# Kernel optimization log

Measured on AMD Instinct MI355X. Metric: run time of the kernel, lower is better.

## Reference

```python
import jax, jax.numpy as jnp
import numpy as np

N = 4096      # mesh nodes (seq len)
D = 512       # input_dim_nodes / hidden_size
F = 512       # ffn_hidden_size (hidden_dim)
NH = 4        # num_attention_heads
HD = D // NH  # head dim = 128
L = 2         # processor_layers
EPS = 1e-5
SCALE = 1.0 / float(np.sqrt(HD))
NEG = -1e9


def setup_inputs() -> dict:
    key = jax.random.key(0)
    ks = jax.random.split(key, 16)
    nfeat = jax.random.normal(ks[0], (N, D), jnp.float32)
    # sparse graph adjacency mask: True = masked out (TE 'arbitrary' convention)
    mask = jax.random.uniform(ks[1], (N, N)) < 0.99
    idx = jnp.arange(N)
    mask = mask.at[idx, idx].set(False)  # keep self-edges unmasked
    s = 0.02
    p = lambda k, shape: jax.random.normal(k, shape, jnp.float32) * s
    return dict(
        nfeat=nfeat, mask=mask,
        ln1_g=jnp.ones((L, D), jnp.float32), ln1_b=jnp.zeros((L, D), jnp.float32),
        wq=p(ks[2], (L, D, D)), bq=p(ks[3], (L, D)),
        wk=p(ks[4], (L, D, D)), bk=p(ks[5], (L, D)),
        wv=p(ks[6], (L, D, D)), bv=p(ks[7], (L, D)),
        wo=p(ks[8], (L, D, D)), bo=p(ks[9], (L, D)),
        ln2_g=jnp.ones((L, D), jnp.float32), ln2_b=jnp.zeros((L, D), jnp.float32),
        fc1_w=p(ks[10], (L, F, D)), fc1_b=p(ks[11], (L, F)),
        fc2_w=p(ks[12], (L, D, F)), fc2_b=p(ks[13], (L, D)),
    )


def _ln(x, g, b):
    mu = x.mean(-1, keepdims=True)
    var = ((x - mu) ** 2).mean(-1, keepdims=True)
    return (x - mu) * jax.lax.rsqrt(var + EPS) * g + b


def reference(nfeat, mask, ln1_g, ln1_b, wq, bq, wk, bk, wv, bv, wo, bo,
              ln2_g, ln2_b, fc1_w, fc1_b, fc2_w, fc2_b):
    def layer(x, p):
        g1, b1, Wq, Bq, Wk, Bk, Wv, Bv, Wo, Bo, g2, b2, W1, B1, W2, B2 = p
        # --- pre-LN self-attention with arbitrary mask ---
        h = _ln(x, g1, b1)                                  # [N, D]
        q = (h @ Wq.T + Bq).reshape(N, NH, HD)
        k = (h @ Wk.T + Bk).reshape(N, NH, HD)
        v = (h @ Wv.T + Bv).reshape(N, NH, HD)
        scores = jnp.einsum('qhd,khd->hqk', q, k) * SCALE   # [NH, N, N]
        scores = jnp.where(mask[None], NEG, scores)
        attn = jax.nn.softmax(scores, axis=-1)
        o = jnp.einsum('hqk,khd->qhd', attn, v).reshape(N, D)
        x = x + o @ Wo.T + Bo
        # --- pre-LN MLP ---
        h2 = _ln(x, g2, b2)
        m = jax.nn.gelu(h2 @ W1.T + B1, approximate=False) @ W2.T + B2
        return x + m, None

    xs = (ln1_g, ln1_b, wq, bq, wk, bk, wv, bv, wo, bo,
          ln2_g, ln2_b, fc1_w, fc1_b, fc2_w, fc2_b)
    out, _ = jax.lax.scan(layer, nfeat, xs)
    return out
```

## Files before the change

### kernel.cpp

```cpp
#include <hip/hip_runtime.h>
#include <math.h>

#define NN 4096
#define DD 512
#define FF 512
#define CAP 256
#define SCALE 0.08838834764831845f

typedef unsigned short u16;
typedef unsigned char u8;
typedef __attribute__((ext_vector_type(8))) short short8;
typedef __attribute__((ext_vector_type(8))) unsigned short ushort8;
typedef __attribute__((ext_vector_type(4))) unsigned short ushort4v;
typedef __attribute__((ext_vector_type(4))) float floatx4;
typedef __attribute__((ext_vector_type(2))) float f32x2;
typedef _Float16 half8v __attribute__((ext_vector_type(8)));

__device__ __forceinline__ float bf2f(u16 u) {
    union { unsigned int i; float f; } x; x.i = ((unsigned int)u) << 16; return x.f;
}
__device__ __forceinline__ u16 f2bf(float f) {
    union { float f; unsigned int i; } x; x.f = f;
    unsigned int r = (x.i + 0x7FFFu + ((x.i >> 16) & 1u)) >> 16;
    return (u16)r;
}
__device__ __forceinline__ u16 f2h(float f) {
    _Float16 h = (_Float16)f;
    union { _Float16 h; u16 u; } x; x.h = h; return x.u;
}
__device__ __forceinline__ u8 f2fp8(float f) {
    union { _Float16 h; u16 u; } x;
    x.h = (_Float16)(f * 0.00390625f);
    u16 h = x.u;
    h = h + 0x3F + ((h >> 7) & 1);
    return (u8)(((h >> 8) & 0x80) | ((h >> 7) & 0x7f));
}
__device__ __forceinline__ float fp82f_sw(u8 b) {
    union { u16 u; _Float16 h; } x;
    x.u = (u16)(((u16)(b & 0x80) << 8) | ((u16)(b & 0x7f) << 7));
    return (float)x.h * 256.0f;
}
__device__ __forceinline__ void gld_lds16(const void* g, void* l) {
    __builtin_amdgcn_global_load_lds((const __attribute__((address_space(1))) void*)g,
                                     (__attribute__((address_space(3))) void*)l, 16, 0, 0);
}

struct W6 {
    const float* w[6];
    const float* bq; const float* bk; const float* bv;
};
__global__ void setup_kernel(W6 wp, u16* __restrict__ dst, float* __restrict__ bcat,
                             const int* __restrict__ mask, int* __restrict__ idx,
                             int* __restrict__ cnt) {
    __shared__ int c;
    if (blockIdx.x >= 192) {
        int row = blockIdx.x - 192;
        if (threadIdx.x == 0) c = 0;
        __syncthreads();
        const int4* mrow = (const int4*)(mask + (size_t)row * NN);
        for (int j4 = threadIdx.x; j4 < NN / 4; j4 += blockDim.x) {
            int4 m4 = mrow[j4];
            int base = j4 * 4;
            if (m4.x == 0) idx[row * CAP + atomicAdd(&c, 1)] = base;
            if (m4.y == 0) idx[row * CAP + atomicAdd(&c, 1)] = base + 1;
            if (m4.z == 0) idx[row * CAP + atomicAdd(&c, 1)] = base + 2;
            if (m4.w == 0) idx[row * CAP + atomicAdd(&c, 1)] = base + 3;
        }
        __syncthreads();
        if (threadIdx.x == 0) cnt[row] = (c < CAP) ? c : CAP;
        return;
    }
    int region = blockIdx.x >> 4;
    int layer = region / 6, mat = region - layer * 6;
    const float* src = wp.w[mat] + (size_t)layer * (DD * DD);
    u16* d = dst + (size_t)region * (DD * DD);
    int off = (blockIdx.x & 15) * 16384 + threadIdx.x * 4;
#pragma unroll
    for (int i = 0; i < 16; i++) {
        int e = off + i * 1024;
        float4 f = *(const float4*)&src[e];
        ushort4v u;
        u.x = f2bf(f.x); u.y = f2bf(f.y); u.z = f2bf(f.z); u.w = f2bf(f.w);
        *(ushort4v*)&d[e] = u;
    }
    if (blockIdx.x < 2) {
        int l = blockIdx.x;
        for (int it = 0; it < 6; it++) {
            int j = it * 256 + threadIdx.x;
            int m = j >> 9, col = j & 511;
            const float* bp = (m == 0) ? wp.bq : (m == 1) ? wp.bk : wp.bv;
            bcat[l * 1536 + j] = bp[l * DD + col];
        }
    }
}

__global__ void ln_kernel(const float* __restrict__ x, const float* __restrict__ g,
                          const float* __restrict__ b, u16* __restrict__ out) {
    int wave = threadIdx.x >> 6, lane = threadIdx.x & 63;
    int row = blockIdx.x * 4 + wave;
    const float* xr = x + (size_t)row * DD;
    float4 p0 = *(const float4*)&xr[lane * 8];
    float4 p1 = *(const float4*)&xr[lane * 8 + 4];
    float v[8] = {p0.x, p0.y, p0.z, p0.w, p1.x, p1.y, p1.z, p1.w};
    float s = 0.f;
#pragma unroll
    for (int i = 0; i < 8; i++) s += v[i];
#pragma unroll
    for (int off = 32; off; off >>= 1) s += __shfl_xor(s, off);
    float mu = s * (1.0f / DD);
    float vs = 0.f;
#pragma unroll
    for (int i = 0; i < 8; i++) { float d = v[i] - mu; vs += d * d; }
#pragma unroll
    for (int off = 32; off; off >>= 1) vs += __shfl_xor(vs, off);
    float r = rsqrtf(vs * (1.0f / DD) + 1e-5f);
    float4 g0 = *(const float4*)&g[lane * 8];
    float4 g1 = *(const float4*)&g[lane * 8 + 4];
    float4 b0 = *(const float4*)&b[lane * 8];
    float4 b1 = *(const float4*)&b[lane * 8 + 4];
    float ge[8] = {g0.x, g0.y, g0.z, g0.w, g1.x, g1.y, g1.z, g1.w};
    float be[8] = {b0.x, b0.y, b0.z, b0.w, b1.x, b1.y, b1.z, b1.w};
    ushort8 ov;
#pragma unroll
    for (int i = 0; i < 8; i++) ov[i] = f2bf((v[i] - mu) * r * ge[i] + be[i]);
    *(ushort8*)&out[(size_t)row * DD + lane * 8] = ov;
}

__device__ __forceinline__ float gelu_fast(float val) {
    float z = fabsf(val) * 0.70710678118654752f;
    float tt = __builtin_amdgcn_rcpf(fmaf(0.3275911f, z, 1.0f));
    float p = fmaf(1.061405429f, tt, -1.453152027f);
    p = fmaf(p, tt, 1.421413741f);
    p = fmaf(p, tt, -0.284496736f);
    p = fmaf(p, tt, 0.254829592f);
    p = p * tt * __expf(-z * z);
    float er_ = 1.0f - p;
    float sgn = (val < 0.f) ? -er_ : er_;
    return val * 0.5f * (1.0f + sgn);
}


template <int MODE>
__launch_bounds__(256)
__global__ void gemm_bf16(const u16* __restrict__ A, const u16* __restrict__ B,
                          const float* __restrict__ bias, const float* __restrict__ resIn,
                          float* __restrict__ resOut, u16* __restrict__ outB,
                          int M, int Nout, int K) {
    __shared__ u16 As[2 * 64 * 64];
    __shared__ u16 Bs[2 * 64 * 64];
    const int m0 = blockIdx.y * 64, n0 = blockIdx.x * 64;
    const int t = threadIdx.x;
    const int wave = t >> 6, lane = t & 63;
    const int wm = (wave & 1) * 32, wn = (wave >> 1) * 32;
    const int sr = t >> 3;
    const int sc = ((((t & 7) - (t >> 3)) & 7)) * 8;
    const int fr = lane & 15, g0 = lane >> 4;
    const int er = (lane >> 4) * 4, ec = lane & 15;

    floatx4 acc[2][2] = {};
    const u16* ag0 = A + (size_t)(m0 + sr) * K + sc;
    const u16* ag1 = A + (size_t)(m0 + 32 + sr) * K + sc;
    const u16* bg0 = B + (size_t)(n0 + sr) * K + sc;
    const u16* bg1 = B + (size_t)(n0 + 32 + sr) * K + sc;
    u16* as0 = As + t * 8;
    u16* as1 = As + 32 * 64 + t * 8;
    u16* bs0 = Bs + t * 8;
    u16* bs1 = Bs + 32 * 64 + t * 8;

    float rin[16];
    if (MODE == 2) {
#pragma unroll
        for (int i = 0; i < 2; i++)
#pragma unroll
            for (int j = 0; j < 2; j++)
#pragma unroll
                for (int r = 0; r < 4; r++)
                    rin[(i * 2 + j) * 4 + r] =
                        resIn[(size_t)(m0 + wm + 16 * i + er + r) * Nout + (n0 + wn + 16 * j + ec)];
    }

    auto stage = [&](int buf, int k0) {
        int o = buf * 4096;
        gld_lds16(ag0 + k0, as0 + o);
        gld_lds16(ag1 + k0, as1 + o);
        gld_lds16(bg0 + k0, bs0 + o);
        gld_lds16(bg1 + k0, bs1 + o);
    };

    const int NK = K >> 6;
    stage(0, 0);
    int cur = 0;
    for (int kt = 0; kt < NK; kt++) {
        __syncthreads();
        if (kt + 1 < NK) stage(cur ^ 1, (kt + 1) * 64);
        const u16* Ab = As + cur * 4096;
        const u16* Bb = Bs + cur * 4096;
#pragma unroll
        for (int h = 0; h < 2; h++) {
            const int fo = (((h << 2) + g0 + fr) & 7) << 3;
            short8 af[2], bf[2];
#pragma unroll
            for (int i = 0; i < 2; i++) af[i] = *(const short8*)&Ab[(wm + 16 * i + fr) * 64 + fo];
#pragma unroll
            for (int j = 0; j < 2; j++) bf[j] = *(const short8*)&Bb[(wn + 16 * j + fr) * 64 + fo];
#pragma unroll
            for (int i = 0; i < 2; i++)
#pragma unroll
                for (int j = 0; j < 2; j++)
                    acc[i][j] = __builtin_amdgcn_mfma_f32_16x16x32_bf16(af[i], bf[j], acc[i][j], 0, 0, 0);
        }
        cur ^= 1;
    }

#pragma unroll
    for (int i = 0; i < 2; i++) {
#pragma unroll
        for (int j = 0; j < 2; j++) {
            int col = n0 + wn + 16 * j + ec;
            float bsv = bias[col];
#pragma unroll
            for (int r = 0; r < 4; r++) {
                int row = m0 + wm + 16 * i + er + r;
                float val = acc[i][j][r] + bsv;
                if (MODE == 1) val = gelu_fast(val);
                if (MODE == 2) {
                    resOut[(size_t)row * Nout + col] = rin[(i * 2 + j) * 4 + r] + val;
                } else {
                    outB[(size_t)row * Nout + col] = f2bf(val);
                }
            }
        }
    }
}

__launch_bounds__(256)
__global__ void gemm_qkv(const u16* __restrict__ A, const u16* __restrict__ B,
                         const float* __restrict__ bias, u16* __restrict__ qOut,
                         u8* __restrict__ kv8) {
    __shared__ u16 As[2 * 128 * 64];
    __shared__ u16 Bs[2 * 64 * 64];
    const int m0 = blockIdx.y * 128, n0 = blockIdx.x * 64;
    const int t = threadIdx.x;
    const int wave = t >> 6, lane = t & 63;
    const int wm = (wave & 1) * 64, wn = (wave >> 1) * 32;
    const int sr = t >> 3;
    const int sc = ((((t & 7) - (t >> 3)) & 7)) * 8;
    const int fr = lane & 15, g0 = lane >> 4;

    floatx4 acc[4][2] = {};
    const u16* agp[4];
    u16* asp[4];
#pragma unroll
    for (int u = 0; u < 4; u++) {
        agp[u] = A + (size_t)(m0 + 32 * u + sr) * DD + sc;
        asp[u] = As + u * (32 * 64) + t * 8;
    }
    const u16* bg0 = B + (size_t)(n0 + sr) * DD + sc;
    const u16* bg1 = B + (size_t)(n0 + 32 + sr) * DD + sc;
    u16* bs0 = Bs + t * 8;
    u16* bs1 = Bs + 32 * 64 + t * 8;

    auto stage = [&](int buf, int k0) {
        int oa = buf * 8192, ob = buf * 4096;
#pragma unroll
        for (int u = 0; u < 4; u++) gld_lds16(agp[u] + k0, asp[u] + oa);
        gld_lds16(bg0 + k0, bs0 + ob);
        gld_lds16(bg1 + k0, bs1 + ob);
    };

    stage(0, 0);
    int cur = 0;
    for (int kt = 0; kt < 8; kt++) {
        __syncthreads();
        if (kt + 1 < 8) stage(cur ^ 1, (kt + 1) * 64);
        const u16* Ab = As + cur * 8192;
        const u16* Bb = Bs + cur * 4096;
#pragma unroll
        for (int h = 0; h < 2; h++) {
            const int fo = (((h << 2) + g0 + fr) & 7) << 3;
            short8 af[4], bf[2];
#pragma unroll
            for (int i = 0; i < 4; i++) af[i] = *(const short8*)&Ab[(wm + 16 * i + fr) * 64 + fo];
#pragma unroll
            for (int j = 0; j < 2; j++) bf[j] = *(const short8*)&Bb[(wn + 16 * j + fr) * 64 + fo];
#pragma unroll
            for (int i = 0; i < 4; i++)
#pragma unroll
                for (int j = 0; j < 2; j++)
                    acc[i][j] = __builtin_amdgcn_mfma_f32_16x16x32_bf16(af[i], bf[j], acc[i][j], 0, 0, 0);
        }
        cur ^= 1;
    }

    const int er = (lane >> 4) * 4, ec = lane & 15;
    const int bx = blockIdx.x;
#pragma unroll
    for (int j = 0; j < 2; j++) {
        int col = n0 + wn + 16 * j + ec;
        float bsv = bias[col];
#pragma unroll
        for (int i = 0; i < 4; i++) {
#pragma unroll
            for (int r = 0; r < 4; r++) {
                int row = m0 + wm + 16 * i + er + r;
                float val = acc[i][j][r] + bsv;
                if (bx < 8) {
                    qOut[(size_t)row * 512 + col] = f2h(val);
                } else if (bx < 16) {
                    int cc = col - 512;
                    kv8[(size_t)row * 1024 + 16 * (cc >> 3) + (cc & 7)] = f2fp8(val);
                } else {
                    int cc = col - 1024;
                    kv8[(size_t)row * 1024 + 16 * (cc >> 3) + 8 + (cc & 7)] = f2fp8(val);
                }
            }
        }
    }
}

__global__ void sparse_attn(const u16* __restrict__ q, const u8* __restrict__ kv8,
                            const int* __restrict__ idx, const int* __restrict__ cnt,
                            u16* __restrict__ o) {
    int t = threadIdx.x;
    int wave = t >> 6, lane = t & 63;
    int qslot = wave >> 1, half = wave & 1;
    int qi = blockIdx.x * 4 + qslot;
    __shared__ float obuf[4][64][8];
    __shared__ float sbuf[4][64];
    __shared__ int sidx[4][CAP];

    int c = cnt[qi];
    const int* ir = idx + qi * CAP;
    for (int j = t & 127; j < c; j += 128) sidx[qslot][j] = ir[j];

    half8v qv = *(const half8v*)(q + (size_t)qi * 512 + lane * 8);
    float qf[8];
#pragma unroll
    for (int e = 0; e < 8; e++) qf[e] = (float)qv[e];
    __syncthreads();

    float sum = 0.f, oa[8] = {};
    int j = half;
    int4 kv0, kv1;
    {
        int k0i = (j < c) ? sidx[qslot][j] : 0;
        int k1i = (j + 2 < c) ? sidx[qslot][j + 2] : 0;
        kv0 = *(const int4*)(kv8 + (size_t)k0i * 1024 + lane * 16);
        kv1 = *(const int4*)(kv8 + (size_t)k1i * 1024 + lane * 16);
    }
    while (j < c) {
        int4 kvn;
        {
            int kjn = (j + 4 < c) ? sidx[qslot][j + 4] : 0;
            kvn = *(const int4*)(kv8 + (size_t)kjn * 1024 + lane * 16);
        }
        float kd[8], vd[8];
#if __has_builtin(__builtin_amdgcn_cvt_pk_f32_fp8)
        {
            f32x2 p0 = __builtin_amdgcn_cvt_pk_f32_fp8(kv0.x, false);
            f32x2 p1 = __builtin_amdgcn_cvt_pk_f32_fp8(kv0.x, true);
            f32x2 p2 = __builtin_amdgcn_cvt_pk_f32_fp8(kv0.y, false);
            f32x2 p3 = __builtin_amdgcn_cvt_pk_f32_fp8(kv0.y, true);
            kd[0] = p0.x; kd[1] = p0.y; kd[2] = p1.x; kd[3] = p1.y;
            kd[4] = p2.x; kd[5] = p2.y; kd[6] = p3.x; kd[7] = p3.y;
            f32x2 p4 = __builtin_amdgcn_cvt_pk_f32_fp8(kv0.z, false);
            f32x2 p5 = __builtin_amdgcn_cvt_pk_f32_fp8(kv0.z, true);
            f32x2 p6 = __builtin_amdgcn_cvt_pk_f32_fp8(kv0.w, false);
            f32x2 p7 = __builtin_amdgcn_cvt_pk_f32_fp8(kv0.w, true);
            vd[0] = p4.x; vd[1] = p4.y; vd[2] = p5.x; vd[3] = p5.y;
            vd[4] = p6.x; vd[5] = p6.y; vd[6] = p7.x; vd[7] = p7.y;
        }
#else
        {
            const u8* bp = (const u8*)&kv0;
#pragma unroll
            for (int e = 0; e < 8; e++) { kd[e] = fp82f_sw(bp[e]); vd[e] = fp82f_sw(bp[8 + e]); }
        }
#endif
        float d = 0.f;
#pragma unroll
        for (int e = 0; e < 8; e++) d = fmaf(qf[e], kd[e], d);
        d += __shfl_xor(d, 1);
        d += __shfl_xor(d, 2);
        d += __shfl_xor(d, 4);
        d += __shfl_xor(d, 8);
        float p = __expf(d * SCALE);
        sum += p;
#pragma unroll
        for (int e = 0; e < 8; e++) oa[e] = fmaf(p, vd[e], oa[e]);
        kv0 = kv1;
        kv1 = kvn;
        j += 2;
    }

    if (half == 1) {
#pragma unroll
        for (int e = 0; e < 8; e++) obuf[qslot][lane][e] = oa[e];
        sbuf[qslot][lane] = sum;
    }
    __syncthreads();
    if (half == 0) {
        sum += sbuf[qslot][lane];
        float inv = 1.0f / sum;
        ushort8 ov;
#pragma unroll
        for (int e = 0; e < 8; e++) ov[e] = f2bf((oa[e] + obuf[qslot][lane][e]) * inv);
        *(ushort8*)(o + (size_t)qi * 512 + lane * 8) = ov;
    }
}

extern "C" void kernel_launch(void* const* d_in, const int* in_sizes, int n_in,
                              void* d_out, int out_size, void* d_ws, size_t ws_size,
                              hipStream_t stream) {
    const float* nfeat = (const float*)d_in[0];
    const int*   mask  = (const int*)d_in[1];
    const float* ln1_g = (const float*)d_in[2];
    const float* ln1_b = (const float*)d_in[3];
    const float* bo    = (const float*)d_in[11];
    const float* ln2_g = (const float*)d_in[12];
    const float* ln2_b = (const float*)d_in[13];
    const float* fc1_b = (const float*)d_in[15];
    const float* fc2_b = (const float*)d_in[17];

    const size_t ND = (size_t)NN * DD;
    float* x    = (float*)d_ws;
    u16*   h    = (u16*)(x + ND);
    u16*   q    = h + ND;
    u8*    kv8  = (u8*)(q + ND);
    u16*   o    = (u16*)(kv8 + (size_t)NN * 1024);
    u16*   m1   = o + ND;
    u16*   wc   = m1 + ND;
    float* bcat = (float*)(wc + (size_t)12 * DD * DD);
    int*   idx  = (int*)(bcat + 2 * 1536);
    int*   cnt  = idx + (size_t)NN * CAP;

    W6 w6;
    w6.w[0] = (const float*)d_in[4];  w6.w[1] = (const float*)d_in[6];
    w6.w[2] = (const float*)d_in[8];  w6.w[3] = (const float*)d_in[10];
    w6.w[4] = (const float*)d_in[14]; w6.w[5] = (const float*)d_in[16];
    w6.bq = (const float*)d_in[5]; w6.bk = (const float*)d_in[7]; w6.bv = (const float*)d_in[9];
    setup_kernel<<<192 + NN, 256, 0, stream>>>(w6, wc, bcat, mask, idx, cnt);

    const size_t SS = (size_t)DD * DD;
    for (int l = 0; l < 2; l++) {
        size_t bOff = (size_t)l * DD;
        u16* wl = wc + (size_t)l * 6 * SS;
        const float* xin = (l == 0) ? nfeat : x;
        float* fc2_dst = (l == 1) ? (float*)d_out : x;

        ln_kernel<<<NN / 4, 256, 0, stream>>>(xin, ln1_g + bOff, ln1_b + bOff, h);
        gemm_qkv<<<dim3(24, 32), 256, 0, stream>>>(h, wl, bcat + l * 1536, q, kv8);
        sparse_attn<<<NN / 4, 512, 0, stream>>>(q, kv8, idx, cnt, o);
        gemm_bf16<2><<<dim3(8, 64), 256, 0, stream>>>(o, wl + 3 * SS, bo + bOff,
                                                      xin, x, nullptr, NN, DD, DD);
        ln_kernel<<<NN / 4, 256, 0, stream>>>(x, ln2_g + bOff, ln2_b + bOff, h);
        gemm_bf16<1><<<dim3(8, 64), 256, 0, stream>>>(h, wl + 4 * SS, fc1_b + bOff,
                                                      nullptr, nullptr, m1, NN, FF, DD);
        gemm_bf16<2><<<dim3(8, 64), 256, 0, stream>>>(m1, wl + 5 * SS, fc2_b + bOff,
                                                      x, fc2_dst, nullptr, NN, DD, FF);
    }
}
```

Before: 281.4 us.

## Fuse LayerNorm into GEMM prologues using row statistics accumulated in epilogues

Removes the standalone LayerNorm kernels. Per-row sum and sum-of-squares are now computed in the setup kernel for the input and atomically accumulated in the residual GEMM epilogues. The QKV and FC1 GEMMs then normalize fp32 activations on the fly while staging the A tile into LDS, which removes the bf16 h round trip and two launches per layer. In exchange, the A tile moves from async global-to-LDS loads to register loads at twice the bytes, the epilogues gain LDS reductions and atomics, and one-pass variance (E[x²]-mu²) may lose some precision.

```diff
diff --git a/kernel.cpp b/kernel.cpp
--- a/kernel.cpp
+++ b/kernel.cpp
@@ -43,87 +43,6 @@
 __device__ __forceinline__ void gld_lds16(const void* g, void* l) {
     __builtin_amdgcn_global_load_lds((const __attribute__((address_space(1))) void*)g,
                                      (__attribute__((address_space(3))) void*)l, 16, 0, 0);
-}
-
-struct W6 {
-    const float* w[6];
-    const float* bq; const float* bk; const float* bv;
-};
-__global__ void setup_kernel(W6 wp, u16* __restrict__ dst, float* __restrict__ bcat,
-                             const int* __restrict__ mask, int* __restrict__ idx,
-                             int* __restrict__ cnt) {
-    __shared__ int c;
-    if (blockIdx.x >= 192) {
-        int row = blockIdx.x - 192;
-        if (threadIdx.x == 0) c = 0;
-        __syncthreads();
-        const int4* mrow = (const int4*)(mask + (size_t)row * NN);
-        for (int j4 = threadIdx.x; j4 < NN / 4; j4 += blockDim.x) {
-            int4 m4 = mrow[j4];
-            int base = j4 * 4;
-            if (m4.x == 0) idx[row * CAP + atomicAdd(&c, 1)] = base;
-            if (m4.y == 0) idx[row * CAP + atomicAdd(&c, 1)] = base + 1;
-            if (m4.z == 0) idx[row * CAP + atomicAdd(&c, 1)] = base + 2;
-            if (m4.w == 0) idx[row * CAP + atomicAdd(&c, 1)] = base + 3;
-        }
-        __syncthreads();
-        if (threadIdx.x == 0) cnt[row] = (c < CAP) ? c : CAP;
-        return;
-    }
-    int region = blockIdx.x >> 4;
-    int layer = region / 6, mat = region - layer * 6;
-    const float* src = wp.w[mat] + (size_t)layer * (DD * DD);
-    u16* d = dst + (size_t)region * (DD * DD);
-    int off = (blockIdx.x & 15) * 16384 + threadIdx.x * 4;
-#pragma unroll
-    for (int i = 0; i < 16; i++) {
-        int e = off + i * 1024;
-        float4 f = *(const float4*)&src[e];
-        ushort4v u;
-        u.x = f2bf(f.x); u.y = f2bf(f.y); u.z = f2bf(f.z); u.w = f2bf(f.w);
-        *(ushort4v*)&d[e] = u;
-    }
-    if (blockIdx.x < 2) {
-        int l = blockIdx.x;
-        for (int it = 0; it < 6; it++) {
-            int j = it * 256 + threadIdx.x;
-            int m = j >> 9, col = j & 511;
-            const float* bp = (m == 0) ? wp.bq : (m == 1) ? wp.bk : wp.bv;
-            bcat[l * 1536 + j] = bp[l * DD + col];
-        }
-    }
-}
-
-__global__ void ln_kernel(const float* __restrict__ x, const float* __restrict__ g,
-                          const float* __restrict__ b, u16* __restrict__ out) {
-    int wave = threadIdx.x >> 6, lane = threadIdx.x & 63;
-    int row = blockIdx.x * 4 + wave;
-    const float* xr = x + (size_t)row * DD;
-    float4 p0 = *(const float4*)&xr[lane * 8];
-    float4 p1 = *(const float4*)&xr[lane * 8 + 4];
-    float v[8] = {p0.x, p0.y, p0.z, p0.w, p1.x, p1.y, p1.z, p1.w};
-    float s = 0.f;
-#pragma unroll
-    for (int i = 0; i < 8; i++) s += v[i];
-#pragma unroll
-    for (int off = 32; off; off >>= 1) s += __shfl_xor(s, off);
-    float mu = s * (1.0f / DD);
-    float vs = 0.f;
-#pragma unroll
-    for (int i = 0; i < 8; i++) { float d = v[i] - mu; vs += d * d; }
-#pragma unroll
-    for (int off = 32; off; off >>= 1) vs += __shfl_xor(vs, off);
-    float r = rsqrtf(vs * (1.0f / DD) + 1e-5f);
-    float4 g0 = *(const float4*)&g[lane * 8];
-    float4 g1 = *(const float4*)&g[lane * 8 + 4];
-    float4 b0 = *(const float4*)&b[lane * 8];
-    float4 b1 = *(const float4*)&b[lane * 8 + 4];
-    float ge[8] = {g0.x, g0.y, g0.z, g0.w, g1.x, g1.y, g1.z, g1.w};
-    float be[8] = {b0.x, b0.y, b0.z, b0.w, b1.x, b1.y, b1.z, b1.w};
-    ushort8 ov;
-#pragma unroll
-    for (int i = 0; i < 8; i++) ov[i] = f2bf((v[i] - mu) * r * ge[i] + be[i]);
-    *(ushort8*)&out[(size_t)row * DD + lane * 8] = ov;
 }
 
 __device__ __forceinline__ float gelu_fast(float val) {
@@ -139,13 +58,84 @@
     return val * 0.5f * (1.0f + sgn);
 }
 
-
-template <int MODE>
+struct W6 {
+    const float* w[6];
+    const float* bq; const float* bk; const float* bv;
+};
+__global__ void setup_kernel(W6 wp, u16* __restrict__ dst, float* __restrict__ bcat,
+                             const int* __restrict__ mask, int* __restrict__ idx,
+                             int* __restrict__ cnt, const float* __restrict__ nfeat,
+                             float* __restrict__ st) {
+    __shared__ int c;
+    const int bid = blockIdx.x;
+    if (bid >= 192 + NN) {
+        int wave = threadIdx.x >> 6, lane = threadIdx.x & 63;
+        int row = (bid - 192 - NN) * 4 + wave;
+        const float* xr = nfeat + (size_t)row * DD + lane * 8;
+        float4 a = *(const float4*)xr;
+        float4 b4 = *(const float4*)(xr + 4);
+        float v[8] = {a.x, a.y, a.z, a.w, b4.x, b4.y, b4.z, b4.w};
+        float s1 = 0.f, s2 = 0.f;
+#pragma unroll
+        for (int e = 0; e < 8; e++) { s1 += v[e]; s2 += v[e] * v[e]; }
+#pragma unroll
+        for (int off = 32; off; off >>= 1) { s1 += __shfl_xor(s1, off); s2 += __shfl_xor(s2, off); }
+        if (lane == 0) { st[row * 2] = s1; st[row * 2 + 1] = s2; }
+        return;
+    }
+    if (bid >= 192) {
+        int row = bid - 192;
+        if (threadIdx.x == 0) c = 0;
+        __syncthreads();
+        const int4* mrow = (const int4*)(mask + (size_t)row * NN);
+        for (int j4 = threadIdx.x; j4 < NN / 4; j4 += blockDim.x) {
+            int4 m4 = mrow[j4];
+            int base = j4 * 4;
+            if (m4.x == 0) idx[row * CAP + atomicAdd(&c, 1)] = base;
+            if (m4.y == 0) idx[row * CAP + atomicAdd(&c, 1)] = base + 1;
+            if (m4.z == 0) idx[row * CAP + atomicAdd(&c, 1)] = base + 2;
+            if (m4.w == 0) idx[row * CAP + atomicAdd(&c, 1)] = base + 3;
+        }
+        __syncthreads();
+        if (threadIdx.x == 0) cnt[row] = (c < CAP) ? c : CAP;
+        return;
+    }
+    int region = bid >> 4;
+    int layer = region / 6, mat = region - layer * 6;
+    const float* src = wp.w[mat] + (size_t)layer * (DD * DD);
+    u16* d = dst + (size_t)region * (DD * DD);
+    int off = (bid & 15) * 16384 + threadIdx.x * 4;
+#pragma unroll
+    for (int i = 0; i < 16; i++) {
+        int e = off + i * 1024;
+        float4 f = *(const float4*)&src[e];
+        ushort4v u;
+        u.x = f2bf(f.x); u.y = f2bf(f.y); u.z = f2bf(f.z); u.w = f2bf(f.w);
+        *(ushort4v*)&d[e] = u;
+    }
+    if (bid < 2) {
+        int l = bid;
+        for (int it = 0; it < 6; it++) {
+            int j = it * 256 + threadIdx.x;
+            int m = j >> 9, col = j & 511;
+            const float* bp = (m == 0) ? wp.bq : (m == 1) ? wp.bk : wp.bv;
+            bcat[l * 1536 + j] = bp[l * DD + col];
+        }
+    }
+    if (bid == 2 || bid == 3) {
+        float* z = st + 8192;
+        int base = (bid - 2) * 256 + threadIdx.x;
+#pragma unroll
+        for (int i = 0; i < 48; i++) z[base + i * 512] = 0.0f;
+    }
+}
+
+
 __launch_bounds__(256)
-__global__ void gemm_bf16(const u16* __restrict__ A, const u16* __restrict__ B,
-                          const float* __restrict__ bias, const float* __restrict__ resIn,
-                          float* __restrict__ resOut, u16* __restrict__ outB,
-                          int M, int Nout, int K) {
+__global__ void gemm_res(const u16* __restrict__ A, const u16* __restrict__ B,
+                         const float* __restrict__ bias, const float* __restrict__ resIn,
+                         float* __restrict__ resOut, float* __restrict__ statsOut,
+                         int Nout, int K) {
     __shared__ u16 As[2 * 64 * 64];
     __shared__ u16 Bs[2 * 64 * 64];
     const int m0 = blockIdx.y * 64, n0 = blockIdx.x * 64;
@@ -168,16 +158,14 @@
     u16* bs1 = Bs + 32 * 64 + t * 8;
 
     float rin[16];
-    if (MODE == 2) {
-#pragma unroll
-        for (int i = 0; i < 2; i++)
-#pragma unroll
-            for (int j = 0; j < 2; j++)
-#pragma unroll
-                for (int r = 0; r < 4; r++)
-                    rin[(i * 2 + j) * 4 + r] =
-                        resIn[(size_t)(m0 + wm + 16 * i + er + r) * Nout + (n0 + wn + 16 * j + ec)];
-    }
+#pragma unroll
+    for (int i = 0; i < 2; i++)
+#pragma unroll
+        for (int j = 0; j < 2; j++)
+#pragma unroll
+            for (int r = 0; r < 4; r++)
+                rin[(i * 2 + j) * 4 + r] =
+                    resIn[(size_t)(m0 + wm + 16 * i + er + r) * Nout + (n0 + wn + 16 * j + ec)];
 
     auto stage = [&](int buf, int k0) {
         int o = buf * 4096;
@@ -212,6 +200,7 @@
         cur ^= 1;
     }
 
+    float outv[16];
 #pragma unroll
     for (int i = 0; i < 2; i++) {
 #pragma unroll
@@ -221,22 +210,161 @@
 #pragma unroll
             for (int r = 0; r < 4; r++) {
                 int row = m0 + wm + 16 * i + er + r;
-                float val = acc[i][j][r] + bsv;
-                if (MODE == 1) val = gelu_fast(val);
-                if (MODE == 2) {
-                    resOut[(size_t)row * Nout + col] = rin[(i * 2 + j) * 4 + r] + val;
-                } else {
-                    outB[(size_t)row * Nout + col] = f2bf(val);
-                }
+                float val = rin[(i * 2 + j) * 4 + r] + acc[i][j][r] + bsv;
+                outv[(i * 2 + j) * 4 + r] = val;
+                resOut[(size_t)row * Nout + col] = val;
             }
         }
     }
+
+    if (statsOut) {
+        __syncthreads();
+        float* Ls = (float*)As;
+#pragma unroll
+        for (int i = 0; i < 2; i++)
+#pragma unroll
+            for (int j = 0; j < 2; j++)
+#pragma unroll
+                for (int r = 0; r < 4; r++)
+                    Ls[(wm + 16 * i + er + r) * 64 + (wn + 16 * j + ec)] = outv[(i * 2 + j) * 4 + r];
+        __syncthreads();
+        if (t < 64) {
+            float s1 = 0.f, s2 = 0.f;
+            for (int c0 = 0; c0 < 64; c0++) {
+                int cc = (c0 + t) & 63;
+                float v = Ls[t * 64 + cc];
+                s1 += v; s2 += v * v;
+            }
+            atomicAdd(&statsOut[(size_t)(m0 + t) * 2], s1);
+            atomicAdd(&statsOut[(size_t)(m0 + t) * 2 + 1], s2);
+        }
+    }
 }
 
 __launch_bounds__(256)
-__global__ void gemm_qkv(const u16* __restrict__ A, const u16* __restrict__ B,
-                         const float* __restrict__ bias, u16* __restrict__ qOut,
-                         u8* __restrict__ kv8) {
+__global__ void gemm_ln_gelu(const float* __restrict__ X, const float* __restrict__ stats,
+                             const float* __restrict__ lg, const float* __restrict__ lb,
+                             const u16* __restrict__ B, const float* __restrict__ bias,
+                             u16* __restrict__ outB) {
+    __shared__ u16 As[2 * 64 * 64];
+    __shared__ u16 Bs[2 * 64 * 64];
+    const int m0 = blockIdx.y * 64, n0 = blockIdx.x * 64;
+    const int t = threadIdx.x;
+    const int wave = t >> 6, lane = t & 63;
+    const int wm = (wave & 1) * 32, wn = (wave >> 1) * 32;
+    const int sr = t >> 3;
+    const int sc = ((((t & 7) - (t >> 3)) & 7)) * 8;
+    const int fr = lane & 15, g0 = lane >> 4;
+
+    floatx4 acc[2][2] = {};
+    const float* xp0 = X + (size_t)(m0 + sr) * DD + sc;
+    const float* xp1 = X + (size_t)(m0 + 32 + sr) * DD + sc;
+    float mu0, r0, mu1, r1;
+    {
+        int ra = m0 + sr, rb = m0 + 32 + sr;
+        float s1 = stats[ra * 2], s2 = stats[ra * 2 + 1];
+        mu0 = s1 * (1.0f / DD);
+        r0 = rsqrtf(s2 * (1.0f / DD) - mu0 * mu0 + 1e-5f);
+        s1 = stats[rb * 2]; s2 = stats[rb * 2 + 1];
+        mu1 = s1 * (1.0f / DD);
+        r1 = rsqrtf(s2 * (1.0f / DD) - mu1 * mu1 + 1e-5f);
+    }
+    const u16* bg0 = B + (size_t)(n0 + sr) * DD + sc;
+    const u16* bg1 = B + (size_t)(n0 + 32 + sr) * DD + sc;
+    u16* as0 = As + t * 8;
+    u16* as1 = As + 32 * 64 + t * 8;
+    u16* bs0 = Bs + t * 8;
+    u16* bs1 = Bs + 32 * 64 + t * 8;
+
+    float4 xa0, xb0, xa1, xb1, ga, gb2, ba, bb2;
+    auto ldx = [&](int k0) {
+        xa0 = *(const float4*)&xp0[k0];
+        xb0 = *(const float4*)&xp0[k0 + 4];
+        xa1 = *(const float4*)&xp1[k0];
+        xb1 = *(const float4*)&xp1[k0 + 4];
+        ga  = *(const float4*)&lg[k0 + sc];
+        gb2 = *(const float4*)&lg[k0 + sc + 4];
+        ba  = *(const float4*)&lb[k0 + sc];
+        bb2 = *(const float4*)&lb[k0 + sc + 4];
+    };
+    auto stA = [&](int buf) {
+        int o_ = buf * 4096;
+        ushort8 h0, h1;
+        h0[0] = f2bf((xa0.x - mu0) * r0 * ga.x + ba.x);
+        h0[1] = f2bf((xa0.y - mu0) * r0 * ga.y + ba.y);
+        h0[2] = f2bf((xa0.z - mu0) * r0 * ga.z + ba.z);
+        h0[3] = f2bf((xa0.w - mu0) * r0 * ga.w + ba.w);
+        h0[4] = f2bf((xb0.x - mu0) * r0 * gb2.x + bb2.x);
+        h0[5] = f2bf((xb0.y - mu0) * r0 * gb2.y + bb2.y);
+        h0[6] = f2bf((xb0.z - mu0) * r0 * gb2.z + bb2.z);
+        h0[7] = f2bf((xb0.w - mu0) * r0 * gb2.w + bb2.w);
+        h1[0] = f2bf((xa1.x - mu1) * r1 * ga.x + ba.x);
+        h1[1] = f2bf((xa1.y - mu1) * r1 * ga.y + ba.y);
+        h1[2] = f2bf((xa1.z - mu1) * r1 * ga.z + ba.z);
+        h1[3] = f2bf((xa1.w - mu1) * r1 * ga.w + ba.w);
+        h1[4] = f2bf((xb1.x - mu1) * r1 * gb2.x + bb2.x);
+        h1[5] = f2bf((xb1.y - mu1) * r1 * gb2.y + bb2.y);
+        h1[6] = f2bf((xb1.z - mu1) * r1 * gb2.z + bb2.z);
+        h1[7] = f2bf((xb1.w - mu1) * r1 * gb2.w + bb2.w);
+        *(ushort8*)(as0 + o_) = h0;
+        *(ushort8*)(as1 + o_) = h1;
+    };
+    auto stB = [&](int buf, int k0) {
+        int o_ = buf * 4096;
+        gld_lds16(bg0 + k0, bs0 + o_);
+        gld_lds16(bg1 + k0, bs1 + o_);
+    };
+
+    ldx(0);
+    stB(0, 0);
+    stA(0);
+    int cur = 0;
+    for (int kt = 0; kt < 8; kt++) {
+        __syncthreads();
+        bool more = (kt < 7);
+        if (more) { stB(cur ^ 1, (kt + 1) * 64); ldx((kt + 1) * 64); }
+        const u16* Ab = As + cur * 4096;
+        const u16* Bb = Bs + cur * 4096;
+#pragma unroll
+        for (int h = 0; h < 2; h++) {
+            const int fo = (((h << 2) + g0 + fr) & 7) << 3;
+            short8 af[2], bf[2];
+#pragma unroll
+            for (int i = 0; i < 2; i++) af[i] = *(const short8*)&Ab[(wm + 16 * i + fr) * 64 + fo];
+#pragma unroll
+            for (int j = 0; j < 2; j++) bf[j] = *(const short8*)&Bb[(wn + 16 * j + fr) * 64 + fo];
+#pragma unroll
+            for (int i = 0; i < 2; i++)
+#pragma unroll
+                for (int j = 0; j < 2; j++)
+                    acc[i][j] = __builtin_amdgcn_mfma_f32_16x16x32_bf16(af[i], bf[j], acc[i][j], 0, 0, 0);
+        }
+        if (more) stA(cur ^ 1);
+        cur ^= 1;
+    }
+
+    const int er = (lane >> 4) * 4, ec = lane & 15;
+#pragma unroll
+    for (int i = 0; i < 2; i++) {
+#pragma unroll
+        for (int j = 0; j < 2; j++) {
+            int col = n0 + wn + 16 * j + ec;
+            float bsv = bias[col];
+#pragma unroll
+            for (int r = 0; r < 4; r++) {
+                int row = m0 + wm + 16 * i + er + r;
+                float val = gelu_fast(acc[i][j][r] + bsv);
+                outB[(size_t)row * FF + col] = f2bf(val);
+            }
+        }
+    }
+}
+
+__launch_bounds__(256)
+__global__ void gemm_qkv_ln(const float* __restrict__ X, const float* __restrict__ stats,
+                            const float* __restrict__ lg, const float* __restrict__ lb,
+                            const u16* __restrict__ B, const float* __restrict__ bias,
+                            u16* __restrict__ qOut, u8* __restrict__ kv8) {
     __shared__ u16 As[2 * 128 * 64];
     __shared__ u16 Bs[2 * 64 * 64];
     const int m0 = blockIdx.y * 128, n0 = blockIdx.x * 64;
@@ -248,11 +376,17 @@
     const int fr = lane & 15, g0 = lane >> 4;
 
     floatx4 acc[4][2] = {};
-    const u16* agp[4];
+    const float* xp[4];
+    float mu_[4], rr_[4];
     u16* asp[4];
 #pragma unroll
     for (int u = 0; u < 4; u++) {
-        agp[u] = A + (size_t)(m0 + 32 * u + sr) * DD + sc;
+        int row = m0 + 32 * u + sr;
+        xp[u] = X + (size_t)row * DD + sc;
+        float s1 = stats[row * 2], s2 = stats[row * 2 + 1];
+        float m = s1 * (1.0f / DD);
+        mu_[u] = m;
+        rr_[u] = rsqrtf(s2 * (1.0f / DD) - m * m + 1e-5f);
         asp[u] = As + u * (32 * 64) + t * 8;
     }
     const u16* bg0 = B + (size_t)(n0 + sr) * DD + sc;
@@ -260,19 +394,48 @@
     u16* bs0 = Bs + t * 8;
     u16* bs1 = Bs + 32 * 64 + t * 8;
 
-    auto stage = [&](int buf, int k0) {
-        int oa = buf * 8192, ob = buf * 4096;
-#pragma unroll
-        for (int u = 0; u < 4; u++) gld_lds16(agp[u] + k0, asp[u] + oa);
-        gld_lds16(bg0 + k0, bs0 + ob);
-        gld_lds16(bg1 + k0, bs1 + ob);
+    float4 xa[4], xb[4], ga, gb2, ba, bb2;
+    auto ldx = [&](int k0) {
+#pragma unroll
+        for (int u = 0; u < 4; u++) {
+            xa[u] = *(const float4*)&xp[u][k0];
+            xb[u] = *(const float4*)&xp[u][k0 + 4];
+        }
+        ga  = *(const float4*)&lg[k0 + sc];
+        gb2 = *(const float4*)&lg[k0 + sc + 4];
+        ba  = *(const float4*)&lb[k0 + sc];
+        bb2 = *(const float4*)&lb[k0 + sc + 4];
     };
-
-    stage(0, 0);
+    auto stA = [&](int buf) {
+        int o_ = buf * 8192;
+#pragma unroll
+        for (int u = 0; u < 4; u++) {
+            ushort8 hv;
+            hv[0] = f2bf((xa[u].x - mu_[u]) * rr_[u] * ga.x + ba.x);
+            hv[1] = f2bf((xa[u].y - mu_[u]) * rr_[u] * ga.y + ba.y);
+            hv[2] = f2bf((xa[u].z - mu_[u]) * rr_[u] * ga.z + ba.z);
+            hv[3] = f2bf((xa[u].w - mu_[u]) * rr_[u] * ga.w + ba.w);
+            hv[4] = f2bf((xb[u].x - mu_[u]) * rr_[u] * gb2.x + bb2.x);
+            hv[5] = f2bf((xb[u].y - mu_[u]) * rr_[u] * gb2.y + bb2.y);
+            hv[6] = f2bf((xb[u].z - mu_[u]) * rr_[u] * gb2.z + bb2.z);
+            hv[7] = f2bf((xb[u].w - mu_[u]) * rr_[u] * gb2.w + bb2.w);
+            *(ushort8*)(asp[u] + o_) = hv;
+        }
+    };
+    auto stB = [&](int buf, int k0) {
+        int o_ = buf * 4096;
+        gld_lds16(bg0 + k0, bs0 + o_);
+        gld_lds16(bg1 + k0, bs1 + o_);
+    };
+
+    ldx(0);
+    stB(0, 0);
+    stA(0);
     int cur = 0;
     for (int kt = 0; kt < 8; kt++) {
         __syncthreads();
-        if (kt + 1 < 8) stage(cur ^ 1, (kt + 1) * 64);
+        bool more = (kt < 7);
+        if (more) { stB(cur ^ 1, (kt + 1) * 64); ldx((kt + 1) * 64); }
         const u16* Ab = As + cur * 8192;
         const u16* Bb = Bs + cur * 4096;
 #pragma unroll
@@ -289,6 +452,7 @@
                 for (int j = 0; j < 2; j++)
                     acc[i][j] = __builtin_amdgcn_mfma_f32_16x16x32_bf16(af[i], bf[j], acc[i][j], 0, 0, 0);
         }
+        if (more) stA(cur ^ 1);
         cur ^= 1;
     }
 
@@ -424,14 +588,14 @@
 
     const size_t ND = (size_t)NN * DD;
     float* x    = (float*)d_ws;
-    u16*   h    = (u16*)(x + ND);
-    u16*   q    = h + ND;
+    u16*   q    = (u16*)(x + ND);
     u8*    kv8  = (u8*)(q + ND);
     u16*   o    = (u16*)(kv8 + (size_t)NN * 1024);
     u16*   m1   = o + ND;
     u16*   wc   = m1 + ND;
     float* bcat = (float*)(wc + (size_t)12 * DD * DD);
-    int*   idx  = (int*)(bcat + 2 * 1536);
+    float* st   = bcat + 2 * 1536;
+    int*   idx  = (int*)(st + 4 * 8192);
     int*   cnt  = idx + (size_t)NN * CAP;
 
     W6 w6;
@@ -439,7 +603,7 @@
     w6.w[2] = (const float*)d_in[8];  w6.w[3] = (const float*)d_in[10];
     w6.w[4] = (const float*)d_in[14]; w6.w[5] = (const float*)d_in[16];
     w6.bq = (const float*)d_in[5]; w6.bk = (const float*)d_in[7]; w6.bv = (const float*)d_in[9];
-    setup_kernel<<<192 + NN, 256, 0, stream>>>(w6, wc, bcat, mask, idx, cnt);
+    setup_kernel<<<192 + NN + NN / 4, 256, 0, stream>>>(w6, wc, bcat, mask, idx, cnt, nfeat, st);
 
     const size_t SS = (size_t)DD * DD;
     for (int l = 0; l < 2; l++) {
@@ -447,16 +611,18 @@
         u16* wl = wc + (size_t)l * 6 * SS;
         const float* xin = (l == 0) ? nfeat : x;
         float* fc2_dst = (l == 1) ? (float*)d_out : x;
-
-        ln_kernel<<<NN / 4, 256, 0, stream>>>(xin, ln1_g + bOff, ln1_b + bOff, h);
-        gemm_qkv<<<dim3(24, 32), 256, 0, stream>>>(h, wl, bcat + l * 1536, q, kv8);
+        float* st_ln1 = st + (l == 0 ? 0 : 2) * 8192;
+        float* st_ln2 = st + (l == 0 ? 1 : 3) * 8192;
+
+        gemm_qkv_ln<<<dim3(24, 32), 256, 0, stream>>>(xin, st_ln1, ln1_g + bOff, ln1_b + bOff,
+                                                      wl, bcat + l * 1536, q, kv8);
         sparse_attn<<<NN / 4, 512, 0, stream>>>(q, kv8, idx, cnt, o);
-        gemm_bf16<2><<<dim3(8, 64), 256, 0, stream>>>(o, wl + 3 * SS, bo + bOff,
-                                                      xin, x, nullptr, NN, DD, DD);
-        ln_kernel<<<NN / 4, 256, 0, stream>>>(x, ln2_g + bOff, ln2_b + bOff, h);
-        gemm_bf16<1><<<dim3(8, 64), 256, 0, stream>>>(h, wl + 4 * SS, fc1_b + bOff,
-                                                      nullptr, nullptr, m1, NN, FF, DD);
-        gemm_bf16<2><<<dim3(8, 64), 256, 0, stream>>>(m1, wl + 5 * SS, fc2_b + bOff,
-                                                      x, fc2_dst, nullptr, NN, DD, FF);
-    }
-}
+        gemm_res<<<dim3(8, 64), 256, 0, stream>>>(o, wl + 3 * SS, bo + bOff,
+                                                  xin, x, st_ln2, DD, DD);
+        gemm_ln_gelu<<<dim3(8, 64), 256, 0, stream>>>(x, st_ln2, ln2_g + bOff, ln2_b + bOff,
+                                                      wl + 4 * SS, fc1_b + bOff, m1);
+        gemm_res<<<dim3(8, 64), 256, 0, stream>>>(m1, wl + 5 * SS, fc2_b + bOff,
+                                                  x, fc2_dst, (l == 0) ? (st + 2 * 8192) : nullptr,
+                                                  DD, FF);
+    }
+}
```

Result: slower. 307.5 us (+9.3%).

## Split K across two thread groups per block in dense GEMMs with LDS reduction

Applied to the files above, without the earlier changes.

The dense GEMM kernels (QKV, output projection, FC1, FC2) now launch 512 threads per block. Two 256-thread groups each process half of the K=512 dimension, and their partial accumulators are reduced through shared memory before the epilogue. The aim is more waves per output tile and better latency hiding on these small-K GEMMs. In exchange, the QKV kernel drops its double-buffered prefetch in favour of two barriers per step, shared memory per block grows, and half the threads sit idle during the epilogue.

```diff
diff --git a/kernel.cpp b/kernel.cpp
--- a/kernel.cpp
+++ b/kernel.cpp
@@ -43,6 +43,19 @@
 __device__ __forceinline__ void gld_lds16(const void* g, void* l) {
     __builtin_amdgcn_global_load_lds((const __attribute__((address_space(1))) void*)g,
                                      (__attribute__((address_space(3))) void*)l, 16, 0, 0);
+}
+
+__device__ __forceinline__ float gelu_fast(float val) {
+    float z = fabsf(val) * 0.70710678118654752f;
+    float tt = __builtin_amdgcn_rcpf(fmaf(0.3275911f, z, 1.0f));
+    float p = fmaf(1.061405429f, tt, -1.453152027f);
+    p = fmaf(p, tt, 1.421413741f);
+    p = fmaf(p, tt, -0.284496736f);
+    p = fmaf(p, tt, 0.254829592f);
+    p = p * tt * __expf(-z * z);
+    float er_ = 1.0f - p;
+    float sgn = (val < 0.f) ? -er_ : er_;
+    return val * 0.5f * (1.0f + sgn);
 }
 
 struct W6 {
@@ -126,49 +139,35 @@
     *(ushort8*)&out[(size_t)row * DD + lane * 8] = ov;
 }
 
-__device__ __forceinline__ float gelu_fast(float val) {
-    float z = fabsf(val) * 0.70710678118654752f;
-    float tt = __builtin_amdgcn_rcpf(fmaf(0.3275911f, z, 1.0f));
-    float p = fmaf(1.061405429f, tt, -1.453152027f);
-    p = fmaf(p, tt, 1.421413741f);
-    p = fmaf(p, tt, -0.284496736f);
-    p = fmaf(p, tt, 0.254829592f);
-    p = p * tt * __expf(-z * z);
-    float er_ = 1.0f - p;
-    float sgn = (val < 0.f) ? -er_ : er_;
-    return val * 0.5f * (1.0f + sgn);
-}
-
 
 template <int MODE>
-__launch_bounds__(256)
-__global__ void gemm_bf16(const u16* __restrict__ A, const u16* __restrict__ B,
-                          const float* __restrict__ bias, const float* __restrict__ resIn,
-                          float* __restrict__ resOut, u16* __restrict__ outB,
-                          int M, int Nout, int K) {
-    __shared__ u16 As[2 * 64 * 64];
-    __shared__ u16 Bs[2 * 64 * 64];
+__launch_bounds__(512)
+__global__ void gemm_fc(const u16* __restrict__ A, const u16* __restrict__ B,
+                        const float* __restrict__ bias, const float* __restrict__ resIn,
+                        float* __restrict__ resOut, u16* __restrict__ outB) {
+    __shared__ __align__(16) u8 smem[65536];
     const int m0 = blockIdx.y * 64, n0 = blockIdx.x * 64;
     const int t = threadIdx.x;
-    const int wave = t >> 6, lane = t & 63;
+    const int grp = t >> 8;
+    const int tg = t & 255;
+    const int wave = tg >> 6, lane = t & 63;
     const int wm = (wave & 1) * 32, wn = (wave >> 1) * 32;
-    const int sr = t >> 3;
-    const int sc = ((((t & 7) - (t >> 3)) & 7)) * 8;
+    const int sr = tg >> 3;
+    const int sc = ((((tg & 7) - (tg >> 3)) & 7)) * 8;
     const int fr = lane & 15, g0 = lane >> 4;
     const int er = (lane >> 4) * 4, ec = lane & 15;
+    const int kbase = grp * 256;
 
     floatx4 acc[2][2] = {};
-    const u16* ag0 = A + (size_t)(m0 + sr) * K + sc;
-    const u16* ag1 = A + (size_t)(m0 + 32 + sr) * K + sc;
-    const u16* bg0 = B + (size_t)(n0 + sr) * K + sc;
-    const u16* bg1 = B + (size_t)(n0 + 32 + sr) * K + sc;
-    u16* as0 = As + t * 8;
-    u16* as1 = As + 32 * 64 + t * 8;
-    u16* bs0 = Bs + t * 8;
-    u16* bs1 = Bs + 32 * 64 + t * 8;
+    const u16* ag0 = A + (size_t)(m0 + sr) * 512 + kbase + sc;
+    const u16* ag1 = A + (size_t)(m0 + 32 + sr) * 512 + kbase + sc;
+    const u16* bg0 = B + (size_t)(n0 + sr) * 512 + kbase + sc;
+    const u16* bg1 = B + (size_t)(n0 + 32 + sr) * 512 + kbase + sc;
+    u16* asg = (u16*)(smem + grp * 32768);
+    u16* bsg = (u16*)(smem + grp * 32768 + 16384);
 
     float rin[16];
-    if (MODE == 2) {
+    if (MODE == 2 && grp == 0) {
 #pragma unroll
         for (int i = 0; i < 2; i++)
 #pragma unroll
@@ -176,25 +175,25 @@
 #pragma unroll
                 for (int r = 0; r < 4; r++)
                     rin[(i * 2 + j) * 4 + r] =
-                        resIn[(size_t)(m0 + wm + 16 * i + er + r) * Nout + (n0 + wn + 16 * j + ec)];
+                        resIn[(size_t)(m0 + wm + 16 * i + er + r) * 512 + (n0 + wn + 16 * j + ec)];
     }
 
     auto stage = [&](int buf, int k0) {
-        int o = buf * 4096;
-        gld_lds16(ag0 + k0, as0 + o);
-        gld_lds16(ag1 + k0, as1 + o);
-        gld_lds16(bg0 + k0, bs0 + o);
-        gld_lds16(bg1 + k0, bs1 + o);
+        u16* a_ = asg + buf * 4096;
+        u16* b_ = bsg + buf * 4096;
+        gld_lds16(ag0 + k0, a_ + tg * 8);
+        gld_lds16(ag1 + k0, a_ + 2048 + tg * 8);
+        gld_lds16(bg0 + k0, b_ + tg * 8);
+        gld_lds16(bg1 + k0, b_ + 2048 + tg * 8);
     };
 
-    const int NK = K >> 6;
     stage(0, 0);
     int cur = 0;
-    for (int kt = 0; kt < NK; kt++) {
+    for (int kt = 0; kt < 4; kt++) {
         __syncthreads();
-        if (kt + 1 < NK) stage(cur ^ 1, (kt + 1) * 64);
-        const u16* Ab = As + cur * 4096;
-        const u16* Bb = Bs + cur * 4096;
+        if (kt < 3) stage(cur ^ 1, (kt + 1) * 64);
+        const u16* Ab = asg + cur * 4096;
+        const u16* Bb = bsg + cur * 4096;
 #pragma unroll
         for (int h = 0; h < 2; h++) {
             const int fo = (((h << 2) + g0 + fr) & 7) << 3;
@@ -212,106 +211,132 @@
         cur ^= 1;
     }
 
-#pragma unroll
-    for (int i = 0; i < 2; i++) {
+    __syncthreads();
+    float* red = (float*)smem;
+    if (grp == 1) {
+#pragma unroll
+        for (int i = 0; i < 2; i++)
+#pragma unroll
+            for (int j = 0; j < 2; j++)
+#pragma unroll
+                for (int r = 0; r < 4; r++)
+                    red[(wm + 16 * i + er + r) * 65 + (wn + 16 * j + ec)] = acc[i][j][r];
+    }
+    __syncthreads();
+    if (grp == 0) {
 #pragma unroll
         for (int j = 0; j < 2; j++) {
             int col = n0 + wn + 16 * j + ec;
             float bsv = bias[col];
 #pragma unroll
-            for (int r = 0; r < 4; r++) {
-                int row = m0 + wm + 16 * i + er + r;
-                float val = acc[i][j][r] + bsv;
-                if (MODE == 1) val = gelu_fast(val);
-                if (MODE == 2) {
-                    resOut[(size_t)row * Nout + col] = rin[(i * 2 + j) * 4 + r] + val;
-                } else {
-                    outB[(size_t)row * Nout + col] = f2bf(val);
+            for (int i = 0; i < 2; i++) {
+#pragma unroll
+                for (int r = 0; r < 4; r++) {
+                    int row = m0 + wm + 16 * i + er + r;
+                    float val = acc[i][j][r] + bsv +
+                                red[(wm + 16 * i + er + r) * 65 + (wn + 16 * j + ec)];
+                    if (MODE == 1) {
+                        outB[(size_t)row * 512 + col] = f2bf(gelu_fast(val));
+                    } else {
+                        resOut[(size_t)row * 512 + col] = rin[(i * 2 + j) * 4 + r] + val;
+                    }
                 }
             }
         }
     }
 }
 
-__launch_bounds__(256)
+__launch_bounds__(512)
 __global__ void gemm_qkv(const u16* __restrict__ A, const u16* __restrict__ B,
                          const float* __restrict__ bias, u16* __restrict__ qOut,
                          u8* __restrict__ kv8) {
-    __shared__ u16 As[2 * 128 * 64];
-    __shared__ u16 Bs[2 * 64 * 64];
+    __shared__ __align__(16) u8 smem[49152];
     const int m0 = blockIdx.y * 128, n0 = blockIdx.x * 64;
     const int t = threadIdx.x;
-    const int wave = t >> 6, lane = t & 63;
+    const int grp = t >> 8;
+    const int tg = t & 255;
+    const int wave = tg >> 6, lane = t & 63;
     const int wm = (wave & 1) * 64, wn = (wave >> 1) * 32;
-    const int sr = t >> 3;
-    const int sc = ((((t & 7) - (t >> 3)) & 7)) * 8;
+    const int sr = tg >> 3;
+    const int sc = ((((tg & 7) - (tg >> 3)) & 7)) * 8;
     const int fr = lane & 15, g0 = lane >> 4;
+    const int er = (lane >> 4) * 4, ec = lane & 15;
+    const int kbase = grp * 256;
 
     floatx4 acc[4][2] = {};
     const u16* agp[4];
+    u16* asg = (u16*)(smem + grp * 24576);
+    u16* bsg = asg + 8192;
     u16* asp[4];
 #pragma unroll
     for (int u = 0; u < 4; u++) {
-        agp[u] = A + (size_t)(m0 + 32 * u + sr) * DD + sc;
-        asp[u] = As + u * (32 * 64) + t * 8;
-    }
-    const u16* bg0 = B + (size_t)(n0 + sr) * DD + sc;
-    const u16* bg1 = B + (size_t)(n0 + 32 + sr) * DD + sc;
-    u16* bs0 = Bs + t * 8;
-    u16* bs1 = Bs + 32 * 64 + t * 8;
-
-    auto stage = [&](int buf, int k0) {
-        int oa = buf * 8192, ob = buf * 4096;
-#pragma unroll
-        for (int u = 0; u < 4; u++) gld_lds16(agp[u] + k0, asp[u] + oa);
-        gld_lds16(bg0 + k0, bs0 + ob);
-        gld_lds16(bg1 + k0, bs1 + ob);
+        agp[u] = A + (size_t)(m0 + 32 * u + sr) * DD + kbase + sc;
+        asp[u] = asg + u * 2048 + tg * 8;
+    }
+    const u16* bg0 = B + (size_t)(n0 + sr) * DD + kbase + sc;
+    const u16* bg1 = B + (size_t)(n0 + 32 + sr) * DD + kbase + sc;
+
+    auto stage = [&](int k0) {
+#pragma unroll
+        for (int u = 0; u < 4; u++) gld_lds16(agp[u] + k0, asp[u]);
+        gld_lds16(bg0 + k0, bsg + tg * 8);
+        gld_lds16(bg1 + k0, bsg + 2048 + tg * 8);
     };
 
-    stage(0, 0);
-    int cur = 0;
-    for (int kt = 0; kt < 8; kt++) {
+    for (int kt = 0; kt < 4; kt++) {
         __syncthreads();
-        if (kt + 1 < 8) stage(cur ^ 1, (kt + 1) * 64);
-        const u16* Ab = As + cur * 8192;
-        const u16* Bb = Bs + cur * 4096;
+        stage(kt * 64);
+        __syncthreads();
 #pragma unroll
         for (int h = 0; h < 2; h++) {
             const int fo = (((h << 2) + g0 + fr) & 7) << 3;
             short8 af[4], bf[2];
 #pragma unroll
-            for (int i = 0; i < 4; i++) af[i] = *(const short8*)&Ab[(wm + 16 * i + fr) * 64 + fo];
-#pragma unroll
-            for (int j = 0; j < 2; j++) bf[j] = *(const short8*)&Bb[(wn + 16 * j + fr) * 64 + fo];
+            for (int i = 0; i < 4; i++) af[i] = *(const short8*)&asg[(wm + 16 * i + fr) * 64 + fo];
+#pragma unroll
+            for (int j = 0; j < 2; j++) bf[j] = *(const short8*)&bsg[(wn + 16 * j + fr) * 64 + fo];
 #pragma unroll
             for (int i = 0; i < 4; i++)
 #pragma unroll
                 for (int j = 0; j < 2; j++)
                     acc[i][j] = __builtin_amdgcn_mfma_f32_16x16x32_bf16(af[i], bf[j], acc[i][j], 0, 0, 0);
         }
-        cur ^= 1;
-    }
-
-    const int er = (lane >> 4) * 4, ec = lane & 15;
-    const int bx = blockIdx.x;
-#pragma unroll
-    for (int j = 0; j < 2; j++) {
-        int col = n0 + wn + 16 * j + ec;
-        float bsv = bias[col];
-#pragma unroll
-        for (int i = 0; i < 4; i++) {
-#pragma unroll
-            for (int r = 0; r < 4; r++) {
-                int row = m0 + wm + 16 * i + er + r;
-                float val = acc[i][j][r] + bsv;
-                if (bx < 8) {
-                    qOut[(size_t)row * 512 + col] = f2h(val);
-                } else if (bx < 16) {
-                    int cc = col - 512;
-                    kv8[(size_t)row * 1024 + 16 * (cc >> 3) + (cc & 7)] = f2fp8(val);
-                } else {
-                    int cc = col - 1024;
-                    kv8[(size_t)row * 1024 + 16 * (cc >> 3) + 8 + (cc & 7)] = f2fp8(val);
+    }
+
+    __syncthreads();
+    float* red = (float*)smem;
+    if (grp == 1) {
+#pragma unroll
+        for (int i = 0; i < 4; i++)
+#pragma unroll
+            for (int j = 0; j < 2; j++)
+#pragma unroll
+                for (int r = 0; r < 4; r++)
+                    red[(wm + 16 * i + er + r) * 65 + (wn + 16 * j + ec)] = acc[i][j][r];
+    }
+    __syncthreads();
+    if (grp == 0) {
+        const int bx = blockIdx.x;
+#pragma unroll
+        for (int j = 0; j < 2; j++) {
+            int col = n0 + wn + 16 * j + ec;
+            float bsv = bias[col];
+#pragma unroll
+            for (int i = 0; i < 4; i++) {
+#pragma unroll
+                for (int r = 0; r < 4; r++) {
+                    int row = m0 + wm + 16 * i + er + r;
+                    float val = acc[i][j][r] + bsv +
+                                red[(wm + 16 * i + er + r) * 65 + (wn + 16 * j + ec)];
+                    if (bx < 8) {
+                        qOut[(size_t)row * 512 + col] = f2h(val);
+                    } else if (bx < 16) {
+                        int cc = col - 512;
+                        kv8[(size_t)row * 1024 + 16 * (cc >> 3) + (cc & 7)] = f2fp8(val);
+                    } else {
+                        int cc = col - 1024;
+                        kv8[(size_t)row * 1024 + 16 * (cc >> 3) + 8 + (cc & 7)] = f2fp8(val);
+                    }
                 }
             }
         }
@@ -449,14 +474,14 @@
         float* fc2_dst = (l == 1) ? (float*)d_out : x;
 
         ln_kernel<<<NN / 4, 256, 0, stream>>>(xin, ln1_g + bOff, ln1_b + bOff, h);
-        gemm_qkv<<<dim3(24, 32), 256, 0, stream>>>(h, wl, bcat + l * 1536, q, kv8);
+        gemm_qkv<<<dim3(24, 32), 512, 0, stream>>>(h, wl, bcat + l * 1536, q, kv8);
         sparse_attn<<<NN / 4, 512, 0, stream>>>(q, kv8, idx, cnt, o);
-        gemm_bf16<2><<<dim3(8, 64), 256, 0, stream>>>(o, wl + 3 * SS, bo + bOff,
-                                                      xin, x, nullptr, NN, DD, DD);
+        gemm_fc<2><<<dim3(8, 64), 512, 0, stream>>>(o, wl + 3 * SS, bo + bOff,
+                                                    xin, x, nullptr);
         ln_kernel<<<NN / 4, 256, 0, stream>>>(x, ln2_g + bOff, ln2_b + bOff, h);
-        gemm_bf16<1><<<dim3(8, 64), 256, 0, stream>>>(h, wl + 4 * SS, fc1_b + bOff,
-                                                      nullptr, nullptr, m1, NN, FF, DD);
-        gemm_bf16<2><<<dim3(8, 64), 256, 0, stream>>>(m1, wl + 5 * SS, fc2_b + bOff,
-                                                      x, fc2_dst, nullptr, NN, DD, FF);
-    }
-}
+        gemm_fc<1><<<dim3(8, 64), 512, 0, stream>>>(h, wl + 4 * SS, fc1_b + bOff,
+                                                    nullptr, nullptr, m1);
+        gemm_fc<2><<<dim3(8, 64), 512, 0, stream>>>(m1, wl + 5 * SS, fc2_b + bOff,
+                                                    x, fc2_dst, nullptr);
+    }
+}
```

Result: no change. 282.3 us (+0.3%).
